# Kernel tuning notes

Hardware: AMD Instinct MI355X
Metric: run time of the kernel (lower is better)

Reference implementation:

```python
import jax, jax.numpy as jnp
import numpy as np

B, S, D_IN, D_OUT = 8, 2048, 1024, 1024


def setup_inputs() -> dict:
    key = jax.random.key(0)
    ks = jax.random.split(key, 9)
    sc = 1.0 / np.sqrt(D_IN)
    return {
        "in_k": jax.random.normal(ks[0], (B, S, D_IN), jnp.float32),
        "in_q": jax.random.normal(ks[1], (B, S, D_IN), jnp.float32),
        "in_v": jax.random.normal(ks[2], (B, S, D_IN), jnp.float32),
        "Wk": jax.random.normal(ks[3], (D_IN, D_OUT), jnp.float32) * sc,
        "bk": jax.random.normal(ks[4], (D_OUT,), jnp.float32) * sc,
        "Wq": jax.random.normal(ks[5], (D_IN, D_OUT), jnp.float32) * sc,
        "bq": jax.random.normal(ks[6], (D_OUT,), jnp.float32) * sc,
        "Wv": jax.random.normal(ks[7], (D_IN, D_OUT), jnp.float32) * sc,
        "bv": jax.random.normal(ks[8], (D_OUT,), jnp.float32) * sc,
    }


def reference(in_k, in_q, in_v, Wk, bk, Wq, bq, Wv, bv):
    k = in_k @ Wk + bk  # [B,S,D]
    q = in_q @ Wq + bq
    v = in_v @ Wv + bv
    scale = 1.0 / jnp.sqrt(jnp.asarray(D_OUT, q.dtype))
    scores = jnp.einsum("bqd,bkd->bqk", q, k) * scale  # [B,S,S]
    attn = jax.nn.softmax(scores, axis=-1)
    return jnp.einsum("bqk,bkd->bqd", attn, v)
```

## Files before the change

kernel.cpp:

```cpp
#include <hip/hip_runtime.h>
#include <hip/hip_bf16.h>
#include <stdint.h>

typedef __bf16 bf16x8 __attribute__((ext_vector_type(8)));
typedef float  f32x4  __attribute__((ext_vector_type(4)));
typedef uint16_t u16x8 __attribute__((ext_vector_type(8)));

__device__ __forceinline__ uint16_t f32_to_bf16(float f) {
    union { float f; uint32_t u; } v; v.f = f;
    uint32_t u = v.u;
    uint32_t r = (u + 0x7FFFu + ((u >> 16) & 1u)) >> 16;
    return (uint16_t)r;
}

__device__ __forceinline__ void gld16(const void* g, void* l) {
    __builtin_amdgcn_global_load_lds(
        (const __attribute__((address_space(1))) void*)g,
        (__attribute__((address_space(3))) void*)l,
        16, 0, 0);
}

__global__ __launch_bounds__(256) void cast3_kernel(
    const float* __restrict__ i0, const float* __restrict__ i1,
    const float* __restrict__ i2, uint16_t* __restrict__ o0,
    uint16_t* __restrict__ o1, uint16_t* __restrict__ o2) {
    const float* in = (blockIdx.z == 0) ? i0 : (blockIdx.z == 1) ? i1 : i2;
    uint16_t* out = (blockIdx.z == 0) ? o0 : (blockIdx.z == 1) ? o1 : o2;
    size_t i = ((size_t)blockIdx.x * 256 + threadIdx.x) * 8;
    float4 a = *(const float4*)(in + i);
    float4 b = *(const float4*)(in + i + 4);
    u16x8 o;
    o[0] = f32_to_bf16(a.x); o[1] = f32_to_bf16(a.y);
    o[2] = f32_to_bf16(a.z); o[3] = f32_to_bf16(a.w);
    o[4] = f32_to_bf16(b.x); o[5] = f32_to_bf16(b.y);
    o[6] = f32_to_bf16(b.z); o[7] = f32_to_bf16(b.w);
    *(u16x8*)(out + i) = o;
}

__global__ __launch_bounds__(256) void wtrans_kernel(
    const float* __restrict__ W0, const float* __restrict__ W1,
    const float* __restrict__ W2, uint16_t* __restrict__ Wt0) {
    const float* W = (blockIdx.z == 0) ? W0 : (blockIdx.z == 1) ? W1 : W2;
    uint16_t* Wt = Wt0 + (size_t)blockIdx.z * 1024 * 1024;
    __shared__ float tile[64][65];
    const int n0 = blockIdx.x * 64, k0 = blockIdx.y * 64;
    const int tx = threadIdx.x & 63, ty0 = threadIdx.x >> 6;
#pragma unroll
    for (int r = 0; r < 16; ++r) {
        int ty = ty0 + r * 4;
        tile[ty][tx] = W[(size_t)(k0 + ty) * 1024 + n0 + tx];
    }
    __syncthreads();
#pragma unroll
    for (int r = 0; r < 16; ++r) {
        int ty = ty0 + r * 4;
        Wt[(size_t)(n0 + ty) * 1024 + k0 + tx] = f32_to_bf16(tile[tx][ty]);
    }
}

__global__ __launch_bounds__(256, 4) void proj3_kernel(
    const uint16_t* __restrict__ Ab, const uint16_t* __restrict__ Bb,
    uint16_t* __restrict__ Cb, uint16_t* __restrict__ Vt,
    const float* __restrict__ b0, const float* __restrict__ b1,
    const float* __restrict__ b2) {
    __shared__ __align__(16) uint16_t As[128 * 32];
    __shared__ __align__(16) uint16_t Bs[128 * 32];

    const int tid  = threadIdx.x;
    const int lane = tid & 63;
    const int wave = tid >> 6;

    const int pidx = blockIdx.x >> 10;
    const int t = blockIdx.x & 1023;
    const int band = t >> 6;
    const int r0 = t & 63;
    const int row0 = (band * 8 + (r0 & 7)) * 128;
    const int col0 = (r0 >> 3) * 128;

    const uint16_t* A = Ab + (size_t)pidx * 16777216;
    const uint16_t* B = Bb + (size_t)pidx * 1048576;
    const float* bias = (pidx == 0) ? b0 : (pidx == 1) ? b1 : b2;

    const int c0 = tid, c1 = tid + 256;
    const int ar0 = c0 >> 2, ak0 = (((c0 & 3) ^ ((ar0 >> 1) & 3))) * 8;
    const int ar1 = c1 >> 2, ak1 = (((c1 & 3) ^ ((ar1 >> 1) & 3))) * 8;

    const int wr = wave >> 1, wc = wave & 1;
    const int mrow = lane & 15;
    const int quad = lane >> 4;
    const int qsw = (quad ^ ((mrow >> 1) & 3)) * 8;

    f32x4 acc[4][4];
#pragma unroll
    for (int i = 0; i < 4; ++i)
#pragma unroll
        for (int j = 0; j < 4; ++j) acc[i][j] = 0.0f;

    for (int k0 = 0; k0 < 1024; k0 += 32) {
        __syncthreads();
        gld16(A + (size_t)(row0 + ar0) * 1024 + k0 + ak0, &As[(size_t)c0 * 8]);
        gld16(A + (size_t)(row0 + ar1) * 1024 + k0 + ak1, &As[(size_t)c1 * 8]);
        gld16(B + (size_t)(col0 + ar0) * 1024 + k0 + ak0, &Bs[(size_t)c0 * 8]);
        gld16(B + (size_t)(col0 + ar1) * 1024 + k0 + ak1, &Bs[(size_t)c1 * 8]);
        __syncthreads();

        bf16x8 af[4], bfj[4];
#pragma unroll
        for (int i = 0; i < 4; ++i)
            af[i] = *(const bf16x8*)&As[(size_t)(wr * 64 + i * 16 + mrow) * 32 + qsw];
#pragma unroll
        for (int j = 0; j < 4; ++j)
            bfj[j] = *(const bf16x8*)&Bs[(size_t)(wc * 64 + j * 16 + mrow) * 32 + qsw];
#pragma unroll
        for (int i = 0; i < 4; ++i)
#pragma unroll
            for (int j = 0; j < 4; ++j)
                acc[i][j] = __builtin_amdgcn_mfma_f32_16x16x32_bf16(
                    af[i], bfj[j], acc[i][j], 0, 0, 0);
    }

    if (pidx < 2) {
        uint16_t* C = Cb + (size_t)pidx * 16777216;
#pragma unroll
        for (int i = 0; i < 4; ++i)
#pragma unroll
            for (int j = 0; j < 4; ++j)
#pragma unroll
                for (int r = 0; r < 4; ++r) {
                    int row = row0 + wr * 64 + i * 16 + quad * 4 + r;
                    int col = col0 + wc * 64 + j * 16 + mrow;
                    C[(size_t)row * 1024 + col] = f32_to_bf16(acc[i][j][r] + bias[col]);
                }
    } else {
#pragma unroll
        for (int i = 0; i < 4; ++i)
#pragma unroll
            for (int j = 0; j < 4; ++j)
#pragma unroll
                for (int r = 0; r < 4; ++r) {
                    int row = row0 + wr * 64 + i * 16 + quad * 4 + r;
                    int col = col0 + wc * 64 + j * 16 + mrow;
                    Vt[((size_t)(row >> 11) * 1024 + col) * 2048 + (row & 2047)] =
                        f32_to_bf16(acc[i][j][r] + bias[col]);
                }
    }
}

template <int EPI>
__global__ __launch_bounds__(256, 4) void gemm_nt_kernel(
    const uint16_t* __restrict__ A, long long lda, long long sAz,
    const uint16_t* __restrict__ B, long long ldb, long long sBz,
    void* __restrict__ Cv, long long ldc, long long sCz,
    int K, float alpha, float* __restrict__ sums, int Z, int tN) {
    __shared__ __align__(16) uint16_t As[128 * 32];
    __shared__ __align__(16) uint16_t Bs[128 * 32];

    const int tid  = threadIdx.x;
    const int lane = tid & 63;
    const int wave = tid >> 6;

    const int bid = blockIdx.x;
    const int z = bid % Z;
    const int t = bid / Z;
    const int bandSz = tN * 8;
    const int band = t / bandSz;
    const int r0 = t - band * bandSz;
    const int row0 = (band * 8 + (r0 & 7)) * 128;
    const int col0 = (r0 >> 3) * 128;

    A += (size_t)z * sAz;
    B += (size_t)z * sBz;

    const int c0 = tid, c1 = tid + 256;
    const int ar0 = c0 >> 2, ak0 = (((c0 & 3) ^ ((ar0 >> 1) & 3))) * 8;
    const int ar1 = c1 >> 2, ak1 = (((c1 & 3) ^ ((ar1 >> 1) & 3))) * 8;

    const int wr = wave >> 1, wc = wave & 1;
    const int mrow = lane & 15;
    const int quad = lane >> 4;
    const int qsw = (quad ^ ((mrow >> 1) & 3)) * 8;

    f32x4 acc[4][4];
#pragma unroll
    for (int i = 0; i < 4; ++i)
#pragma unroll
        for (int j = 0; j < 4; ++j) acc[i][j] = 0.0f;

    for (int k0 = 0; k0 < K; k0 += 32) {
        __syncthreads();
        gld16(A + (size_t)(row0 + ar0) * lda + k0 + ak0, &As[(size_t)c0 * 8]);
        gld16(A + (size_t)(row0 + ar1) * lda + k0 + ak1, &As[(size_t)c1 * 8]);
        gld16(B + (size_t)(col0 + ar0) * ldb + k0 + ak0, &Bs[(size_t)c0 * 8]);
        gld16(B + (size_t)(col0 + ar1) * ldb + k0 + ak1, &Bs[(size_t)c1 * 8]);
        __syncthreads();

        bf16x8 af[4], bfj[4];
#pragma unroll
        for (int i = 0; i < 4; ++i)
            af[i] = *(const bf16x8*)&As[(size_t)(wr * 64 + i * 16 + mrow) * 32 + qsw];
#pragma unroll
        for (int j = 0; j < 4; ++j)
            bfj[j] = *(const bf16x8*)&Bs[(size_t)(wc * 64 + j * 16 + mrow) * 32 + qsw];
#pragma unroll
        for (int i = 0; i < 4; ++i)
#pragma unroll
            for (int j = 0; j < 4; ++j)
                acc[i][j] = __builtin_amdgcn_mfma_f32_16x16x32_bf16(
                    af[i], bfj[j], acc[i][j], 0, 0, 0);
    }

    if (EPI == 1) {
        uint16_t* C = (uint16_t*)Cv + (size_t)z * sCz;
        float rs[4][4];
#pragma unroll
        for (int i = 0; i < 4; ++i)
#pragma unroll
            for (int r = 0; r < 4; ++r) rs[i][r] = 0.0f;
#pragma unroll
        for (int i = 0; i < 4; ++i)
#pragma unroll
            for (int j = 0; j < 4; ++j)
#pragma unroll
                for (int r = 0; r < 4; ++r) {
                    int row = row0 + wr * 64 + i * 16 + quad * 4 + r;
                    int col = col0 + wc * 64 + j * 16 + mrow;
                    float e = __expf(acc[i][j][r] * alpha);
                    C[(size_t)row * ldc + col] = f32_to_bf16(e);
                    rs[i][r] += e;
                }
#pragma unroll
        for (int i = 0; i < 4; ++i)
#pragma unroll
            for (int r = 0; r < 4; ++r) {
                float s = rs[i][r];
                s += __shfl_xor(s, 1, 64);
                s += __shfl_xor(s, 2, 64);
                s += __shfl_xor(s, 4, 64);
                s += __shfl_xor(s, 8, 64);
                if (mrow == 0) {
                    int row = row0 + wr * 64 + i * 16 + quad * 4 + r;
                    atomicAdd(&sums[(size_t)z * 2048 + row], s);
                }
            }
    } else {
        float* C = (float*)Cv + (size_t)z * sCz;
        float inv[4][4];
#pragma unroll
        for (int i = 0; i < 4; ++i)
#pragma unroll
            for (int r = 0; r < 4; ++r) {
                int row = row0 + wr * 64 + i * 16 + quad * 4 + r;
                inv[i][r] = 1.0f / sums[(size_t)z * 2048 + row];
            }
#pragma unroll
        for (int i = 0; i < 4; ++i)
#pragma unroll
            for (int j = 0; j < 4; ++j)
#pragma unroll
                for (int r = 0; r < 4; ++r) {
                    int row = row0 + wr * 64 + i * 16 + quad * 4 + r;
                    int col = col0 + wc * 64 + j * 16 + mrow;
                    C[(size_t)row * ldc + col] = acc[i][j][r] * inv[i][r];
                }
    }
}

extern "C" void kernel_launch(void* const* d_in, const int* in_sizes, int n_in,
                              void* d_out, int out_size, void* d_ws, size_t ws_size,
                              hipStream_t stream) {
    const float* in_k = (const float*)d_in[0];
    const float* in_q = (const float*)d_in[1];
    const float* in_v = (const float*)d_in[2];
    const float* Wk = (const float*)d_in[3];
    const float* bk = (const float*)d_in[4];
    const float* Wq = (const float*)d_in[5];
    const float* bq = (const float*)d_in[6];
    const float* Wv = (const float*)d_in[7];
    const float* bv = (const float*)d_in[8];
    float* out = (float*)d_out;

    char* w = (char*)d_ws;
    uint16_t* Xq  = (uint16_t*)(w + 0);
    uint16_t* Xk  = (uint16_t*)(w + 33554432);
    uint16_t* Xv  = (uint16_t*)(w + 67108864);
    uint16_t* Qb  = (uint16_t*)(w + 100663296);
    uint16_t* Kb  = (uint16_t*)(w + 134217728);
    uint16_t* Vt  = (uint16_t*)(w + 167772160);
    uint16_t* Wqt = (uint16_t*)(w + 201326592);
    uint16_t* Sc  = Xq;
    float*    sums = (float*)Xv;

    wtrans_kernel<<<dim3(16, 16, 3), 256, 0, stream>>>(Wq, Wk, Wv, Wqt);
    cast3_kernel<<<dim3(8192, 1, 3), 256, 0, stream>>>(in_q, in_k, in_v, Xq, Xk, Xv);

    proj3_kernel<<<3072, 256, 0, stream>>>(Xq, Wqt, Qb, Vt, bq, bk, bv);

    hipMemsetAsync(sums, 0, 8 * 2048 * sizeof(float), stream);

    gemm_nt_kernel<1><<<2048, 256, 0, stream>>>(
        Qb, 1024, 2048LL * 1024, Kb, 1024, 2048LL * 1024,
        Sc, 2048, 2048LL * 2048, 1024, 0.03125f, sums, 8, 16);

    gemm_nt_kernel<2><<<1024, 256, 0, stream>>>(
        Sc, 2048, 2048LL * 2048, Vt, 2048, 1024LL * 2048,
        out, 1024, 2048LL * 1024, 2048, 1.0f, sums, 8, 8);
}
```

Before: 535.0 us.

## Rewrite GEMMs as 256x256 double-buffered tiles with interleaved MFMA scheduling

Replaces the 128x128, single-buffered, K=32 GEMM kernels with a shared 256x256 tile core for the projection and both attention GEMMs. The core uses 512 threads, K=64 steps, double-buffered LDS with global_load_lds prefetch, XOR swizzling, and barrier plus setprio phases that interleave LDS reads with MFMA bursts. Block-to-tile mapping is also changed to spread work across XCDs. The goal is higher arithmetic intensity per byte loaded and overlap of memory with compute. The cost is 128KB of LDS and heavy register use, which lowers occupancy, and fewer blocks, which can leave CUs idle.

```diff
diff --git a/kernel.cpp b/kernel.cpp
--- a/kernel.cpp
+++ b/kernel.cpp
@@ -19,6 +19,11 @@
         (__attribute__((address_space(3))) void*)l,
         16, 0, 0);
 }
+
+#define MFMA16 __builtin_amdgcn_mfma_f32_16x16x32_bf16
+#define SBAR   __builtin_amdgcn_s_barrier
+#define SCHED0() __builtin_amdgcn_sched_barrier(0)
+#define PRIO   __builtin_amdgcn_s_setprio
 
 __global__ __launch_bounds__(256) void cast3_kernel(
     const float* __restrict__ i0, const float* __restrict__ i1,
@@ -58,210 +63,240 @@
     }
 }
 
-__global__ __launch_bounds__(256, 4) void proj3_kernel(
+__device__ __forceinline__ void stage_tile(const uint16_t* __restrict__ G,
+                                           int ldg, int k0,
+                                           uint16_t* lds, int tid) {
+    const int r = tid >> 3, ch = tid & 7;
+    const int c = ((ch ^ (r & 7)) << 3);
+#pragma unroll
+    for (int i = 0; i < 4; ++i) {
+        const int row = i * 64 + r;
+        gld16(G + (size_t)row * ldg + k0 + c, lds + i * 4096 + tid * 8);
+    }
+}
+
+__device__ __forceinline__ void gemm_core(const uint16_t* __restrict__ A, int lda,
+                                          const uint16_t* __restrict__ B, int ldb,
+                                          int K, f32x4 (&acc)[8][4]) {
+    __shared__ __align__(16) uint16_t As[2][16384];
+    __shared__ __align__(16) uint16_t Bs[2][16384];
+    const int tid  = threadIdx.x;
+    const int lane = tid & 63;
+    const int wave = tid >> 6;
+    const int wr = wave >> 2, wcn = wave & 3;
+    const int mrow = lane & 15, q = lane >> 4;
+    const int sx = mrow & 7;
+    const int abase = (wr * 128 + mrow) * 64;
+    const int bbase = (wcn * 64 + mrow) * 64;
+    const int c0 = ((q ^ sx) << 3);
+    const int c1 = (((4 + q) ^ sx) << 3);
+
+    stage_tile(A, lda, 0, As[0], tid);
+    stage_tile(B, ldb, 0, Bs[0], tid);
+    __syncthreads();
+
+    const int NT = K >> 6;
+    bf16x8 af[4][2], bA[2][2], bB[2][2];
+    for (int t = 0; t < NT; ++t) {
+        const int cur = t & 1;
+        const uint16_t* as = As[cur];
+        const uint16_t* bs = Bs[cur];
+        const int kn = (t + 1) << 6;
+        const bool pf = (t + 1 < NT);
+
+        if (pf) stage_tile(A, lda, kn, As[cur ^ 1], tid);
+#pragma unroll
+        for (int m = 0; m < 4; ++m) {
+            af[m][0] = *(const bf16x8*)&as[abase + m * 1024 + c0];
+            af[m][1] = *(const bf16x8*)&as[abase + m * 1024 + c1];
+        }
+#pragma unroll
+        for (int n = 0; n < 2; ++n) {
+            bA[n][0] = *(const bf16x8*)&bs[bbase + n * 1024 + c0];
+            bA[n][1] = *(const bf16x8*)&bs[bbase + n * 1024 + c1];
+        }
+        SBAR(); SCHED0();
+        PRIO(1);
+#pragma unroll
+        for (int m = 0; m < 4; ++m)
+#pragma unroll
+            for (int n = 0; n < 2; ++n) {
+                acc[m][n] = MFMA16(af[m][0], bA[n][0], acc[m][n], 0, 0, 0);
+                acc[m][n] = MFMA16(af[m][1], bA[n][1], acc[m][n], 0, 0, 0);
+            }
+        PRIO(0);
+        SBAR(); SCHED0();
+
+        if (pf) stage_tile(B, ldb, kn, Bs[cur ^ 1], tid);
+#pragma unroll
+        for (int n = 0; n < 2; ++n) {
+            bB[n][0] = *(const bf16x8*)&bs[bbase + (n + 2) * 1024 + c0];
+            bB[n][1] = *(const bf16x8*)&bs[bbase + (n + 2) * 1024 + c1];
+        }
+        SBAR(); SCHED0();
+        PRIO(1);
+#pragma unroll
+        for (int m = 0; m < 4; ++m)
+#pragma unroll
+            for (int n = 0; n < 2; ++n) {
+                acc[m][n + 2] = MFMA16(af[m][0], bB[n][0], acc[m][n + 2], 0, 0, 0);
+                acc[m][n + 2] = MFMA16(af[m][1], bB[n][1], acc[m][n + 2], 0, 0, 0);
+            }
+        PRIO(0);
+        SBAR(); SCHED0();
+
+#pragma unroll
+        for (int m = 0; m < 4; ++m) {
+            af[m][0] = *(const bf16x8*)&as[abase + (m + 4) * 1024 + c0];
+            af[m][1] = *(const bf16x8*)&as[abase + (m + 4) * 1024 + c1];
+        }
+        SBAR(); SCHED0();
+        PRIO(1);
+#pragma unroll
+        for (int m = 0; m < 4; ++m)
+#pragma unroll
+            for (int n = 0; n < 2; ++n) {
+                acc[m + 4][n + 2] = MFMA16(af[m][0], bB[n][0], acc[m + 4][n + 2], 0, 0, 0);
+                acc[m + 4][n + 2] = MFMA16(af[m][1], bB[n][1], acc[m + 4][n + 2], 0, 0, 0);
+            }
+#pragma unroll
+        for (int m = 0; m < 4; ++m)
+#pragma unroll
+            for (int n = 0; n < 2; ++n) {
+                acc[m + 4][n] = MFMA16(af[m][0], bA[n][0], acc[m + 4][n], 0, 0, 0);
+                acc[m + 4][n] = MFMA16(af[m][1], bA[n][1], acc[m + 4][n], 0, 0, 0);
+            }
+        PRIO(0);
+        __syncthreads();
+    }
+}
+
+__global__ __launch_bounds__(512, 2) void proj256_kernel(
     const uint16_t* __restrict__ Ab, const uint16_t* __restrict__ Bb,
     uint16_t* __restrict__ Cb, uint16_t* __restrict__ Vt,
     const float* __restrict__ b0, const float* __restrict__ b1,
     const float* __restrict__ b2) {
-    __shared__ __align__(16) uint16_t As[128 * 32];
-    __shared__ __align__(16) uint16_t Bs[128 * 32];
-
-    const int tid  = threadIdx.x;
-    const int lane = tid & 63;
-    const int wave = tid >> 6;
-
-    const int pidx = blockIdx.x >> 10;
-    const int t = blockIdx.x & 1023;
-    const int band = t >> 6;
-    const int r0 = t & 63;
-    const int row0 = (band * 8 + (r0 & 7)) * 128;
-    const int col0 = (r0 >> 3) * 128;
-
-    const uint16_t* A = Ab + (size_t)pidx * 16777216;
-    const uint16_t* B = Bb + (size_t)pidx * 1048576;
+    const int bid = blockIdx.x;
+    const int lg = (bid & 7) * 96 + (bid >> 3);
+    const int pidx = lg >> 8;
+    const int t = lg & 255;
+    const int band = t >> 4;
+    const int Mt = band * 4 + (t & 3);
+    const int Nt = (t >> 2) & 3;
+    const int row0 = Mt * 256, col0 = Nt * 256;
+
+    const uint16_t* A = Ab + (size_t)pidx * 16777216 + (size_t)row0 * 1024;
+    const uint16_t* B = Bb + (size_t)pidx * 1048576 + (size_t)col0 * 1024;
     const float* bias = (pidx == 0) ? b0 : (pidx == 1) ? b1 : b2;
 
-    const int c0 = tid, c1 = tid + 256;
-    const int ar0 = c0 >> 2, ak0 = (((c0 & 3) ^ ((ar0 >> 1) & 3))) * 8;
-    const int ar1 = c1 >> 2, ak1 = (((c1 & 3) ^ ((ar1 >> 1) & 3))) * 8;
-
-    const int wr = wave >> 1, wc = wave & 1;
-    const int mrow = lane & 15;
-    const int quad = lane >> 4;
-    const int qsw = (quad ^ ((mrow >> 1) & 3)) * 8;
-
-    f32x4 acc[4][4];
-#pragma unroll
-    for (int i = 0; i < 4; ++i)
+    f32x4 acc[8][4];
+#pragma unroll
+    for (int i = 0; i < 8; ++i)
 #pragma unroll
         for (int j = 0; j < 4; ++j) acc[i][j] = 0.0f;
 
-    for (int k0 = 0; k0 < 1024; k0 += 32) {
-        __syncthreads();
-        gld16(A + (size_t)(row0 + ar0) * 1024 + k0 + ak0, &As[(size_t)c0 * 8]);
-        gld16(A + (size_t)(row0 + ar1) * 1024 + k0 + ak1, &As[(size_t)c1 * 8]);
-        gld16(B + (size_t)(col0 + ar0) * 1024 + k0 + ak0, &Bs[(size_t)c0 * 8]);
-        gld16(B + (size_t)(col0 + ar1) * 1024 + k0 + ak1, &Bs[(size_t)c1 * 8]);
-        __syncthreads();
-
-        bf16x8 af[4], bfj[4];
-#pragma unroll
-        for (int i = 0; i < 4; ++i)
-            af[i] = *(const bf16x8*)&As[(size_t)(wr * 64 + i * 16 + mrow) * 32 + qsw];
-#pragma unroll
-        for (int j = 0; j < 4; ++j)
-            bfj[j] = *(const bf16x8*)&Bs[(size_t)(wc * 64 + j * 16 + mrow) * 32 + qsw];
-#pragma unroll
-        for (int i = 0; i < 4; ++i)
-#pragma unroll
-            for (int j = 0; j < 4; ++j)
-                acc[i][j] = __builtin_amdgcn_mfma_f32_16x16x32_bf16(
-                    af[i], bfj[j], acc[i][j], 0, 0, 0);
-    }
+    gemm_core(A, 1024, B, 1024, 1024, acc);
+
+    const int tid = threadIdx.x, lane = tid & 63, wave = tid >> 6;
+    const int wr = wave >> 2, wcn = wave & 3;
+    const int mrow = lane & 15, quad = lane >> 4;
+    float bv_[4];
+#pragma unroll
+    for (int n = 0; n < 4; ++n) bv_[n] = bias[col0 + wcn * 64 + n * 16 + mrow];
 
     if (pidx < 2) {
         uint16_t* C = Cb + (size_t)pidx * 16777216;
 #pragma unroll
-        for (int i = 0; i < 4; ++i)
-#pragma unroll
-            for (int j = 0; j < 4; ++j)
+        for (int m = 0; m < 8; ++m)
+#pragma unroll
+            for (int n = 0; n < 4; ++n)
 #pragma unroll
                 for (int r = 0; r < 4; ++r) {
-                    int row = row0 + wr * 64 + i * 16 + quad * 4 + r;
-                    int col = col0 + wc * 64 + j * 16 + mrow;
-                    C[(size_t)row * 1024 + col] = f32_to_bf16(acc[i][j][r] + bias[col]);
+                    int row = row0 + wr * 128 + m * 16 + quad * 4 + r;
+                    int col = col0 + wcn * 64 + n * 16 + mrow;
+                    C[(size_t)row * 1024 + col] = f32_to_bf16(acc[m][n][r] + bv_[n]);
                 }
     } else {
 #pragma unroll
-        for (int i = 0; i < 4; ++i)
-#pragma unroll
-            for (int j = 0; j < 4; ++j)
+        for (int m = 0; m < 8; ++m)
+#pragma unroll
+            for (int n = 0; n < 4; ++n)
 #pragma unroll
                 for (int r = 0; r < 4; ++r) {
-                    int row = row0 + wr * 64 + i * 16 + quad * 4 + r;
-                    int col = col0 + wc * 64 + j * 16 + mrow;
+                    int row = row0 + wr * 128 + m * 16 + quad * 4 + r;
+                    int col = col0 + wcn * 64 + n * 16 + mrow;
                     Vt[((size_t)(row >> 11) * 1024 + col) * 2048 + (row & 2047)] =
-                        f32_to_bf16(acc[i][j][r] + bias[col]);
+                        f32_to_bf16(acc[m][n][r] + bv_[n]);
                 }
     }
 }
 
 template <int EPI>
-__global__ __launch_bounds__(256, 4) void gemm_nt_kernel(
-    const uint16_t* __restrict__ A, long long lda, long long sAz,
-    const uint16_t* __restrict__ B, long long ldb, long long sBz,
-    void* __restrict__ Cv, long long ldc, long long sCz,
-    int K, float alpha, float* __restrict__ sums, int Z, int tN) {
-    __shared__ __align__(16) uint16_t As[128 * 32];
-    __shared__ __align__(16) uint16_t Bs[128 * 32];
-
-    const int tid  = threadIdx.x;
-    const int lane = tid & 63;
-    const int wave = tid >> 6;
-
+__global__ __launch_bounds__(512, 2) void att256_kernel(
+    const uint16_t* __restrict__ Abase, int lda, long long sAz,
+    const uint16_t* __restrict__ Bbase, int ldb, long long sBz,
+    void* __restrict__ Cv, int ldc, long long sCz,
+    int K, float alpha, float* __restrict__ sums, int NtN, int chunk) {
     const int bid = blockIdx.x;
-    const int z = bid % Z;
-    const int t = bid / Z;
-    const int bandSz = tN * 8;
-    const int band = t / bandSz;
-    const int r0 = t - band * bandSz;
-    const int row0 = (band * 8 + (r0 & 7)) * 128;
-    const int col0 = (r0 >> 3) * 128;
-
-    A += (size_t)z * sAz;
-    B += (size_t)z * sBz;
-
-    const int c0 = tid, c1 = tid + 256;
-    const int ar0 = c0 >> 2, ak0 = (((c0 & 3) ^ ((ar0 >> 1) & 3))) * 8;
-    const int ar1 = c1 >> 2, ak1 = (((c1 & 3) ^ ((ar1 >> 1) & 3))) * 8;
-
-    const int wr = wave >> 1, wc = wave & 1;
-    const int mrow = lane & 15;
-    const int quad = lane >> 4;
-    const int qsw = (quad ^ ((mrow >> 1) & 3)) * 8;
-
-    f32x4 acc[4][4];
-#pragma unroll
-    for (int i = 0; i < 4; ++i)
+    const int lg = (bid & 7) * chunk + (bid >> 3);
+    const int z = lg / chunk;
+    const int t = lg % chunk;
+    const int r2 = t & (2 * NtN - 1);
+    const int band = t / (2 * NtN);
+    const int Mt = band * 2 + (r2 & 1);
+    const int Nt = r2 >> 1;
+    const int row0 = Mt * 256, col0 = Nt * 256;
+
+    const uint16_t* A = Abase + (size_t)z * sAz + (size_t)row0 * lda;
+    const uint16_t* B = Bbase + (size_t)z * sBz + (size_t)col0 * ldb;
+
+    f32x4 acc[8][4];
+#pragma unroll
+    for (int i = 0; i < 8; ++i)
 #pragma unroll
         for (int j = 0; j < 4; ++j) acc[i][j] = 0.0f;
 
-    for (int k0 = 0; k0 < K; k0 += 32) {
-        __syncthreads();
-        gld16(A + (size_t)(row0 + ar0) * lda + k0 + ak0, &As[(size_t)c0 * 8]);
-        gld16(A + (size_t)(row0 + ar1) * lda + k0 + ak1, &As[(size_t)c1 * 8]);
-        gld16(B + (size_t)(col0 + ar0) * ldb + k0 + ak0, &Bs[(size_t)c0 * 8]);
-        gld16(B + (size_t)(col0 + ar1) * ldb + k0 + ak1, &Bs[(size_t)c1 * 8]);
-        __syncthreads();
-
-        bf16x8 af[4], bfj[4];
-#pragma unroll
-        for (int i = 0; i < 4; ++i)
-            af[i] = *(const bf16x8*)&As[(size_t)(wr * 64 + i * 16 + mrow) * 32 + qsw];
-#pragma unroll
-        for (int j = 0; j < 4; ++j)
-            bfj[j] = *(const bf16x8*)&Bs[(size_t)(wc * 64 + j * 16 + mrow) * 32 + qsw];
-#pragma unroll
-        for (int i = 0; i < 4; ++i)
-#pragma unroll
-            for (int j = 0; j < 4; ++j)
-                acc[i][j] = __builtin_amdgcn_mfma_f32_16x16x32_bf16(
-                    af[i], bfj[j], acc[i][j], 0, 0, 0);
-    }
+    gemm_core(A, lda, B, ldb, K, acc);
+
+    const int tid = threadIdx.x, lane = tid & 63, wave = tid >> 6;
+    const int wr = wave >> 2, wcn = wave & 3;
+    const int mrow = lane & 15, quad = lane >> 4;
 
     if (EPI == 1) {
         uint16_t* C = (uint16_t*)Cv + (size_t)z * sCz;
-        float rs[4][4];
-#pragma unroll
-        for (int i = 0; i < 4; ++i)
-#pragma unroll
-            for (int r = 0; r < 4; ++r) rs[i][r] = 0.0f;
-#pragma unroll
-        for (int i = 0; i < 4; ++i)
-#pragma unroll
-            for (int j = 0; j < 4; ++j)
-#pragma unroll
-                for (int r = 0; r < 4; ++r) {
-                    int row = row0 + wr * 64 + i * 16 + quad * 4 + r;
-                    int col = col0 + wc * 64 + j * 16 + mrow;
-                    float e = __expf(acc[i][j][r] * alpha);
+#pragma unroll
+        for (int m = 0; m < 8; ++m)
+#pragma unroll
+            for (int r = 0; r < 4; ++r) {
+                int row = row0 + wr * 128 + m * 16 + quad * 4 + r;
+                float s = 0.0f;
+#pragma unroll
+                for (int n = 0; n < 4; ++n) {
+                    int col = col0 + wcn * 64 + n * 16 + mrow;
+                    float e = __expf(acc[m][n][r] * alpha);
                     C[(size_t)row * ldc + col] = f32_to_bf16(e);
-                    rs[i][r] += e;
+                    s += e;
                 }
-#pragma unroll
-        for (int i = 0; i < 4; ++i)
-#pragma unroll
-            for (int r = 0; r < 4; ++r) {
-                float s = rs[i][r];
                 s += __shfl_xor(s, 1, 64);
                 s += __shfl_xor(s, 2, 64);
                 s += __shfl_xor(s, 4, 64);
                 s += __shfl_xor(s, 8, 64);
-                if (mrow == 0) {
-                    int row = row0 + wr * 64 + i * 16 + quad * 4 + r;
-                    atomicAdd(&sums[(size_t)z * 2048 + row], s);
-                }
+                if (mrow == 0) atomicAdd(&sums[(size_t)z * 2048 + row], s);
             }
     } else {
         float* C = (float*)Cv + (size_t)z * sCz;
-        float inv[4][4];
-#pragma unroll
-        for (int i = 0; i < 4; ++i)
+#pragma unroll
+        for (int m = 0; m < 8; ++m)
 #pragma unroll
             for (int r = 0; r < 4; ++r) {
-                int row = row0 + wr * 64 + i * 16 + quad * 4 + r;
-                inv[i][r] = 1.0f / sums[(size_t)z * 2048 + row];
-            }
-#pragma unroll
-        for (int i = 0; i < 4; ++i)
-#pragma unroll
-            for (int j = 0; j < 4; ++j)
-#pragma unroll
-                for (int r = 0; r < 4; ++r) {
-                    int row = row0 + wr * 64 + i * 16 + quad * 4 + r;
-                    int col = col0 + wc * 64 + j * 16 + mrow;
-                    C[(size_t)row * ldc + col] = acc[i][j][r] * inv[i][r];
+                int row = row0 + wr * 128 + m * 16 + quad * 4 + r;
+                float inv = 1.0f / sums[(size_t)z * 2048 + row];
+#pragma unroll
+                for (int n = 0; n < 4; ++n) {
+                    int col = col0 + wcn * 64 + n * 16 + mrow;
+                    C[(size_t)row * ldc + col] = acc[m][n][r] * inv;
                 }
+            }
     }
 }
 
@@ -293,15 +328,15 @@
     wtrans_kernel<<<dim3(16, 16, 3), 256, 0, stream>>>(Wq, Wk, Wv, Wqt);
     cast3_kernel<<<dim3(8192, 1, 3), 256, 0, stream>>>(in_q, in_k, in_v, Xq, Xk, Xv);
 
-    proj3_kernel<<<3072, 256, 0, stream>>>(Xq, Wqt, Qb, Vt, bq, bk, bv);
+    proj256_kernel<<<768, 512, 0, stream>>>(Xq, Wqt, Qb, Vt, bq, bk, bv);
 
     hipMemsetAsync(sums, 0, 8 * 2048 * sizeof(float), stream);
 
-    gemm_nt_kernel<1><<<2048, 256, 0, stream>>>(
+    att256_kernel<1><<<512, 512, 0, stream>>>(
         Qb, 1024, 2048LL * 1024, Kb, 1024, 2048LL * 1024,
-        Sc, 2048, 2048LL * 2048, 1024, 0.03125f, sums, 8, 16);
-
-    gemm_nt_kernel<2><<<1024, 256, 0, stream>>>(
+        Sc, 2048, 2048LL * 2048, 1024, 0.03125f, sums, 8, 64);
+
+    att256_kernel<2><<<256, 512, 0, stream>>>(
         Sc, 2048, 2048LL * 2048, Vt, 2048, 1024LL * 2048,
-        out, 1024, 2048LL * 1024, 2048, 1.0f, sums, 8, 8);
-}
+        out, 1024, 2048LL * 1024, 2048, 1.0f, sums, 4, 32);
+}
```

After: 565.2 us. 1.06x slower.
